# Optimization experiments

Hardware: AMD Instinct MI355X
Metric: run time of the kernel (lower is better)

## Reference

```python
import jax, jax.numpy as jnp
import numpy as np

B, MUL = 512, 64
DIMS = {0: 1, 1: 3, 2: 5}
PAIRS = [(0, 0), (0, 1), (0, 2), (1, 1), (1, 2), (2, 2)]  # l2 >= l1 (filter_symmetric)
LS_OUT = (0, 1, 2)


def _triples():
    for l1, l2 in PAIRS:
        for l3 in range(abs(l1 - l2), l1 + l2 + 1):
            if l3 in LS_OUT:
                yield (l1, l2, l3)


def setup_inputs() -> dict:
    key = jax.random.key(0)
    inp = {}
    for l in LS_OUT:
        key, k = jax.random.split(key)
        inp['x%d' % l] = jax.random.normal(k, (B, MUL, DIMS[l]), dtype=jnp.float32)
    for (l1, l2, l3) in _triples():
        key, k = jax.random.split(key)
        inp['w3j_%d_%d_%d' % (l1, l2, l3)] = jax.random.normal(
            k, (DIMS[l1], DIMS[l2], DIMS[l3]), dtype=jnp.float32) * 0.1
    return inp


def _forward(x, w):
    # ls_rule='full', channel_rule='full', filter_symmetric=True
    out = {l3: [] for l3 in LS_OUT}
    for l1, l2 in PAIRS:
        # outer product over channels and m-components: [B, i*j, 2l1+1, 2l2+1]
        op = jnp.einsum('bim,bjn->bijmn', x[l1], x[l2])
        b, i, j, m, n = op.shape
        op = op.reshape(b, i * j, m, n)
        for l3 in range(abs(l1 - l2), l1 + l2 + 1):
            if l3 in LS_OUT:
                # contract with Clebsch-Gordan / w3j coefficients
                out[l3].append(jnp.einsum('mnM,bimn->biM', w[(l1, l2, l3)], op))
    return tuple(jnp.concatenate(out[l3], axis=1) for l3 in LS_OUT)


def reference(x0, x1, x2,
              w3j_0_0_0, w3j_0_1_1, w3j_0_2_2,
              w3j_1_1_0, w3j_1_1_1, w3j_1_1_2,
              w3j_1_2_1, w3j_1_2_2,
              w3j_2_2_0, w3j_2_2_1, w3j_2_2_2):
    x = {0: x0, 1: x1, 2: x2}
    w = {(0, 0, 0): w3j_0_0_0, (0, 1, 1): w3j_0_1_1, (0, 2, 2): w3j_0_2_2,
         (1, 1, 0): w3j_1_1_0, (1, 1, 1): w3j_1_1_1, (1, 1, 2): w3j_1_1_2,
         (1, 2, 1): w3j_1_2_1, (1, 2, 2): w3j_1_2_2,
         (2, 2, 0): w3j_2_2_0, (2, 2, 1): w3j_2_2_1, (2, 2, 2): w3j_2_2_2}
    return _forward(x, w)
```

## Files before the change

kernel.cpp:

```cpp
#include <hip/hip_runtime.h>


#define OUT1_BASE (512 * 12288)
#define OUT2_BASE (OUT1_BASE + 512 * 49152)

__global__ __launch_bounds__(256) void tp_kernel(
    const float* __restrict__ x0, const float* __restrict__ x1, const float* __restrict__ x2,
    const float* __restrict__ w000, const float* __restrict__ w011, const float* __restrict__ w022,
    const float* __restrict__ w110, const float* __restrict__ w111, const float* __restrict__ w112,
    const float* __restrict__ w121, const float* __restrict__ w122,
    const float* __restrict__ w220, const float* __restrict__ w221, const float* __restrict__ w222,
    float* __restrict__ out)
{
    __shared__ __align__(16) float s_out[8192];

    const int b    = blockIdx.x >> 4;
    const int tile = blockIdx.x & 15;
    const int t    = threadIdx.x;
    const int c    = tile * 256 + t;
    const int i    = c >> 6;
    const int j    = c & 63;

    const float a0 = x0[b * 64 + i];
    const float b0 = x0[b * 64 + j];
    float a1[3], b1[3], a2[5], b2[5];
#pragma unroll
    for (int m = 0; m < 3; ++m) a1[m] = x1[b * 192 + i * 3 + m];
#pragma unroll
    for (int n = 0; n < 3; ++n) b1[n] = x1[b * 192 + j * 3 + n];
#pragma unroll
    for (int m = 0; m < 5; ++m) a2[m] = x2[b * 320 + i * 5 + m];
#pragma unroll
    for (int n = 0; n < 5; ++n) b2[n] = x2[b * 320 + j * 5 + n];

    float* __restrict__ out0 = out + (size_t)b * 12288;

    out0[c] = w000[0] * (a0 * b0);

    {
        float o[3] = {0.f, 0.f, 0.f};
#pragma unroll
        for (int n = 0; n < 3; ++n) {
            const float p = a0 * b1[n];
#pragma unroll
            for (int M = 0; M < 3; ++M) o[M] += w011[n * 3 + M] * p;
        }
#pragma unroll
        for (int M = 0; M < 3; ++M) s_out[0 * 768 + t * 3 + M] = o[M];
    }

    {
        float o[5] = {0.f, 0.f, 0.f, 0.f, 0.f};
#pragma unroll
        for (int n = 0; n < 5; ++n) {
            const float p = a0 * b2[n];
#pragma unroll
            for (int M = 0; M < 5; ++M) o[M] += w022[n * 5 + M] * p;
        }
#pragma unroll
        for (int M = 0; M < 5; ++M) s_out[3072 + 0 * 1280 + t * 5 + M] = o[M];
    }

    {
        float p[9];
#pragma unroll
        for (int m = 0; m < 3; ++m)
#pragma unroll
            for (int n = 0; n < 3; ++n) p[m * 3 + n] = a1[m] * b1[n];

        {
            float o = 0.f;
#pragma unroll
            for (int k = 0; k < 9; ++k) o += w110[k] * p[k];
            out0[4096 + c] = o;
        }
        {
            float o[3] = {0.f, 0.f, 0.f};
#pragma unroll
            for (int k = 0; k < 9; ++k)
#pragma unroll
                for (int M = 0; M < 3; ++M) o[M] += w111[k * 3 + M] * p[k];
#pragma unroll
            for (int M = 0; M < 3; ++M) s_out[1 * 768 + t * 3 + M] = o[M];
        }
        {
            float o[5] = {0.f, 0.f, 0.f, 0.f, 0.f};
#pragma unroll
            for (int k = 0; k < 9; ++k)
#pragma unroll
                for (int M = 0; M < 5; ++M) o[M] += w112[k * 5 + M] * p[k];
#pragma unroll
            for (int M = 0; M < 5; ++M) s_out[3072 + 1 * 1280 + t * 5 + M] = o[M];
        }
    }

    {
        float p[15];
#pragma unroll
        for (int m = 0; m < 3; ++m)
#pragma unroll
            for (int n = 0; n < 5; ++n) p[m * 5 + n] = a1[m] * b2[n];

        {
            float o[3] = {0.f, 0.f, 0.f};
#pragma unroll
            for (int k = 0; k < 15; ++k)
#pragma unroll
                for (int M = 0; M < 3; ++M) o[M] += w121[k * 3 + M] * p[k];
#pragma unroll
            for (int M = 0; M < 3; ++M) s_out[2 * 768 + t * 3 + M] = o[M];
        }
        {
            float o[5] = {0.f, 0.f, 0.f, 0.f, 0.f};
#pragma unroll
            for (int k = 0; k < 15; ++k)
#pragma unroll
                for (int M = 0; M < 5; ++M) o[M] += w122[k * 5 + M] * p[k];
#pragma unroll
            for (int M = 0; M < 5; ++M) s_out[3072 + 2 * 1280 + t * 5 + M] = o[M];
        }
    }

    {
        float p[25];
#pragma unroll
        for (int m = 0; m < 5; ++m)
#pragma unroll
            for (int n = 0; n < 5; ++n) p[m * 5 + n] = a2[m] * b2[n];

        {
            float o = 0.f;
#pragma unroll
            for (int k = 0; k < 25; ++k) o += w220[k] * p[k];
            out0[2 * 4096 + c] = o;
        }
        {
            float o[3] = {0.f, 0.f, 0.f};
#pragma unroll
            for (int k = 0; k < 25; ++k)
#pragma unroll
                for (int M = 0; M < 3; ++M) o[M] += w221[k * 3 + M] * p[k];
#pragma unroll
            for (int M = 0; M < 3; ++M) s_out[3 * 768 + t * 3 + M] = o[M];
        }
        {
            float o[5] = {0.f, 0.f, 0.f, 0.f, 0.f};
#pragma unroll
            for (int k = 0; k < 25; ++k)
#pragma unroll
                for (int M = 0; M < 5; ++M) o[M] += w222[k * 5 + M] * p[k];
#pragma unroll
            for (int M = 0; M < 5; ++M) s_out[3072 + 3 * 1280 + t * 5 + M] = o[M];
        }
    }

    __syncthreads();

    const float4* __restrict__ s4 = (const float4*)s_out;
#pragma unroll
    for (int k = 0; k < 8; ++k) {
        const int fi = k * 256 + t;
        const float4 v = s4[fi];
        int dst;
        if (fi < 768) {
            const int q   = fi / 192;
            const int off = fi % 192;
            dst = OUT1_BASE + b * 49152 + q * 12288 + tile * 768 + 4 * off;
        } else {
            const int r   = fi - 768;
            const int q   = r / 320;
            const int off = r % 320;
            dst = OUT2_BASE + b * 81920 + q * 20480 + tile * 1280 + 4 * off;
        }
        *(float4*)(out + dst) = v;
    }
}

extern "C" void kernel_launch(void* const* d_in, const int* in_sizes, int n_in,
                              void* d_out, int out_size, void* d_ws, size_t ws_size,
                              hipStream_t stream) {
    const float* x0   = (const float*)d_in[0];
    const float* x1   = (const float*)d_in[1];
    const float* x2   = (const float*)d_in[2];
    const float* w000 = (const float*)d_in[3];
    const float* w011 = (const float*)d_in[4];
    const float* w022 = (const float*)d_in[5];
    const float* w110 = (const float*)d_in[6];
    const float* w111 = (const float*)d_in[7];
    const float* w112 = (const float*)d_in[8];
    const float* w121 = (const float*)d_in[9];
    const float* w122 = (const float*)d_in[10];
    const float* w220 = (const float*)d_in[11];
    const float* w221 = (const float*)d_in[12];
    const float* w222 = (const float*)d_in[13];
    float* outp = (float*)d_out;

    dim3 grid(512 * 16);
    dim3 block(256);
    tp_kernel<<<grid, block, 0, stream>>>(x0, x1, x2,
                                          w000, w011, w022, w110, w111, w112,
                                          w121, w122, w220, w221, w222, outp);
}
```

Before: 318.3 us.

## Factor CG contraction through a-side and compute four j outputs per thread

Each thread now computes four consecutive j channels for one i. It first folds the a-vector into the w3j tensor, so that work is shared across the four j values, then contracts with each b-vector. Outputs are written straight to global memory as float4, which removes the shared-memory staging buffer and the barrier. The grid shrinks by four times, and register pressure rises because of the per-path accumulators.

```diff
diff --git a/kernel.cpp b/kernel.cpp
--- a/kernel.cpp
+++ b/kernel.cpp
@@ -3,6 +3,46 @@
 
 #define OUT1_BASE (512 * 12288)
 #define OUT2_BASE (OUT1_BASE + 512 * 49152)
+
+template<int D1, int D2, int D3>
+__device__ __forceinline__ void do_path(const float* __restrict__ w,
+                                        const float* a, const float* bv,
+                                        float* __restrict__ op)
+{
+    float wa[D2 * D3];
+#pragma unroll
+    for (int k = 0; k < D2 * D3; ++k) wa[k] = 0.f;
+#pragma unroll
+    for (int m = 0; m < D1; ++m) {
+        const float am = a[m];
+#pragma unroll
+        for (int n = 0; n < D2; ++n)
+#pragma unroll
+            for (int M = 0; M < D3; ++M)
+                wa[n * D3 + M] += w[(m * D2 + n) * D3 + M] * am;
+    }
+
+    float o[4 * D3];
+#pragma unroll
+    for (int k = 0; k < 4 * D3; ++k) o[k] = 0.f;
+#pragma unroll
+    for (int jj = 0; jj < 4; ++jj)
+#pragma unroll
+        for (int n = 0; n < D2; ++n) {
+            const float bb = bv[jj * D2 + n];
+#pragma unroll
+            for (int M = 0; M < D3; ++M)
+                o[jj * D3 + M] += wa[n * D3 + M] * bb;
+        }
+
+#pragma unroll
+    for (int q = 0; q < D3; ++q) {
+        float4 v;
+        v.x = o[4 * q + 0]; v.y = o[4 * q + 1];
+        v.z = o[4 * q + 2]; v.w = o[4 * q + 3];
+        *(float4*)(op + 4 * q) = v;
+    }
+}
 
 __global__ __launch_bounds__(256) void tp_kernel(
     const float* __restrict__ x0, const float* __restrict__ x1, const float* __restrict__ x2,
@@ -12,168 +52,58 @@
     const float* __restrict__ w220, const float* __restrict__ w221, const float* __restrict__ w222,
     float* __restrict__ out)
 {
-    __shared__ __align__(16) float s_out[8192];
+    const int b   = blockIdx.x >> 2;
+    const int seg = blockIdx.x & 3;
+    const int t   = threadIdx.x;
+    const int c0  = seg * 1024 + t * 4;
+    const int i   = c0 >> 6;
+    const int j0  = c0 & 63;
 
-    const int b    = blockIdx.x >> 4;
-    const int tile = blockIdx.x & 15;
-    const int t    = threadIdx.x;
-    const int c    = tile * 256 + t;
-    const int i    = c >> 6;
-    const int j    = c & 63;
-
-    const float a0 = x0[b * 64 + i];
-    const float b0 = x0[b * 64 + j];
-    float a1[3], b1[3], a2[5], b2[5];
+    const float a0[1] = { x0[b * 64 + i] };
+    float a1[3], a2[5];
 #pragma unroll
     for (int m = 0; m < 3; ++m) a1[m] = x1[b * 192 + i * 3 + m];
 #pragma unroll
-    for (int n = 0; n < 3; ++n) b1[n] = x1[b * 192 + j * 3 + n];
+    for (int m = 0; m < 5; ++m) a2[m] = x2[b * 320 + i * 5 + m];
+
+    float b0v[4], b1v[12], b2v[20];
+    {
+        const float4 v = *(const float4*)(x0 + b * 64 + j0);
+        b0v[0] = v.x; b0v[1] = v.y; b0v[2] = v.z; b0v[3] = v.w;
+    }
 #pragma unroll
-    for (int m = 0; m < 5; ++m) a2[m] = x2[b * 320 + i * 5 + m];
+    for (int k = 0; k < 3; ++k) {
+        const float4 v = *(const float4*)(x1 + b * 192 + j0 * 3 + 4 * k);
+        b1v[4 * k + 0] = v.x; b1v[4 * k + 1] = v.y;
+        b1v[4 * k + 2] = v.z; b1v[4 * k + 3] = v.w;
+    }
 #pragma unroll
-    for (int n = 0; n < 5; ++n) b2[n] = x2[b * 320 + j * 5 + n];
-
-    float* __restrict__ out0 = out + (size_t)b * 12288;
-
-    out0[c] = w000[0] * (a0 * b0);
-
-    {
-        float o[3] = {0.f, 0.f, 0.f};
-#pragma unroll
-        for (int n = 0; n < 3; ++n) {
-            const float p = a0 * b1[n];
-#pragma unroll
-            for (int M = 0; M < 3; ++M) o[M] += w011[n * 3 + M] * p;
-        }
-#pragma unroll
-        for (int M = 0; M < 3; ++M) s_out[0 * 768 + t * 3 + M] = o[M];
+    for (int k = 0; k < 5; ++k) {
+        const float4 v = *(const float4*)(x2 + b * 320 + j0 * 5 + 4 * k);
+        b2v[4 * k + 0] = v.x; b2v[4 * k + 1] = v.y;
+        b2v[4 * k + 2] = v.z; b2v[4 * k + 3] = v.w;
     }
 
-    {
-        float o[5] = {0.f, 0.f, 0.f, 0.f, 0.f};
-#pragma unroll
-        for (int n = 0; n < 5; ++n) {
-            const float p = a0 * b2[n];
-#pragma unroll
-            for (int M = 0; M < 5; ++M) o[M] += w022[n * 5 + M] * p;
-        }
-#pragma unroll
-        for (int M = 0; M < 5; ++M) s_out[3072 + 0 * 1280 + t * 5 + M] = o[M];
-    }
+    float* __restrict__ o0 = out + b * 12288;
+    float* __restrict__ o1 = out + OUT1_BASE + b * 49152;
+    float* __restrict__ o2 = out + OUT2_BASE + b * 81920;
 
-    {
-        float p[9];
-#pragma unroll
-        for (int m = 0; m < 3; ++m)
-#pragma unroll
-            for (int n = 0; n < 3; ++n) p[m * 3 + n] = a1[m] * b1[n];
+    do_path<1, 1, 1>(w000, a0, b0v, o0 + 0 * 4096 + c0);
 
-        {
-            float o = 0.f;
-#pragma unroll
-            for (int k = 0; k < 9; ++k) o += w110[k] * p[k];
-            out0[4096 + c] = o;
-        }
-        {
-            float o[3] = {0.f, 0.f, 0.f};
-#pragma unroll
-            for (int k = 0; k < 9; ++k)
-#pragma unroll
-                for (int M = 0; M < 3; ++M) o[M] += w111[k * 3 + M] * p[k];
-#pragma unroll
-            for (int M = 0; M < 3; ++M) s_out[1 * 768 + t * 3 + M] = o[M];
-        }
-        {
-            float o[5] = {0.f, 0.f, 0.f, 0.f, 0.f};
-#pragma unroll
-            for (int k = 0; k < 9; ++k)
-#pragma unroll
-                for (int M = 0; M < 5; ++M) o[M] += w112[k * 5 + M] * p[k];
-#pragma unroll
-            for (int M = 0; M < 5; ++M) s_out[3072 + 1 * 1280 + t * 5 + M] = o[M];
-        }
-    }
+    do_path<1, 3, 3>(w011, a0, b1v, o1 + 0 * 12288 + c0 * 3);
 
-    {
-        float p[15];
-#pragma unroll
-        for (int m = 0; m < 3; ++m)
-#pragma unroll
-            for (int n = 0; n < 5; ++n) p[m * 5 + n] = a1[m] * b2[n];
+    do_path<1, 5, 5>(w022, a0, b2v, o2 + 0 * 20480 + c0 * 5);
 
-        {
-            float o[3] = {0.f, 0.f, 0.f};
-#pragma unroll
-            for (int k = 0; k < 15; ++k)
-#pragma unroll
-                for (int M = 0; M < 3; ++M) o[M] += w121[k * 3 + M] * p[k];
-#pragma unroll
-            for (int M = 0; M < 3; ++M) s_out[2 * 768 + t * 3 + M] = o[M];
-        }
-        {
-            float o[5] = {0.f, 0.f, 0.f, 0.f, 0.f};
-#pragma unroll
-            for (int k = 0; k < 15; ++k)
-#pragma unroll
-                for (int M = 0; M < 5; ++M) o[M] += w122[k * 5 + M] * p[k];
-#pragma unroll
-            for (int M = 0; M < 5; ++M) s_out[3072 + 2 * 1280 + t * 5 + M] = o[M];
-        }
-    }
+    do_path<3, 3, 1>(w110, a1, b1v, o0 + 1 * 4096 + c0);
+    do_path<3, 3, 3>(w111, a1, b1v, o1 + 1 * 12288 + c0 * 3);
+    do_path<3, 3, 5>(w112, a1, b1v, o2 + 1 * 20480 + c0 * 5);
 
-    {
-        float p[25];
-#pragma unroll
-        for (int m = 0; m < 5; ++m)
-#pragma unroll
-            for (int n = 0; n < 5; ++n) p[m * 5 + n] = a2[m] * b2[n];
+    do_path<3, 5, 3>(w121, a1, b2v, o1 + 2 * 12288 + c0 * 3);
+    do_path<3, 5, 5>(w122, a1, b2v, o2 + 2 * 20480 + c0 * 5);
 
-        {
-            float o = 0.f;
-#pragma unroll
-            for (int k = 0; k < 25; ++k) o += w220[k] * p[k];
-            out0[2 * 4096 + c] = o;
-        }
-        {
-            float o[3] = {0.f, 0.f, 0.f};
-#pragma unroll
-            for (int k = 0; k < 25; ++k)
-#pragma unroll
-                for (int M = 0; M < 3; ++M) o[M] += w221[k * 3 + M] * p[k];
-#pragma unroll
-            for (int M = 0; M < 3; ++M) s_out[3 * 768 + t * 3 + M] = o[M];
-        }
-        {
-            float o[5] = {0.f, 0.f, 0.f, 0.f, 0.f};
-#pragma unroll
-            for (int k = 0; k < 25; ++k)
-#pragma unroll
-                for (int M = 0; M < 5; ++M) o[M] += w222[k * 5 + M] * p[k];
-#pragma unroll
-            for (int M = 0; M < 5; ++M) s_out[3072 + 3 * 1280 + t * 5 + M] = o[M];
-        }
-    }
-
-    __syncthreads();
-
-    const float4* __restrict__ s4 = (const float4*)s_out;
-#pragma unroll
-    for (int k = 0; k < 8; ++k) {
-        const int fi = k * 256 + t;
-        const float4 v = s4[fi];
-        int dst;
-        if (fi < 768) {
-            const int q   = fi / 192;
-            const int off = fi % 192;
-            dst = OUT1_BASE + b * 49152 + q * 12288 + tile * 768 + 4 * off;
-        } else {
-            const int r   = fi - 768;
-            const int q   = r / 320;
-            const int off = r % 320;
-            dst = OUT2_BASE + b * 81920 + q * 20480 + tile * 1280 + 4 * off;
-        }
-        *(float4*)(out + dst) = v;
-    }
+    do_path<5, 5, 1>(w220, a2, b2v, o0 + 2 * 4096 + c0);
+    do_path<5, 5, 3>(w221, a2, b2v, o1 + 3 * 12288 + c0 * 3);
+    do_path<5, 5, 5>(w222, a2, b2v, o2 + 3 * 20480 + c0 * 5);
 }
 
 extern "C" void kernel_launch(void* const* d_in, const int* in_sizes, int n_in,
@@ -195,7 +125,7 @@
     const float* w222 = (const float*)d_in[13];
     float* outp = (float*)d_out;
 
-    dim3 grid(512 * 16);
+    dim3 grid(512 * 4);
     dim3 block(256);
     tp_kernel<<<grid, block, 0, stream>>>(x0, x1, x2,
                                           w000, w011, w022, w110, w111, w112,
```

Result: slower. 358.7 us (+12.7%).
